# Kernel optimization log

Hardware: AMD Instinct MI355X
Metric: run time of the kernel (lower is better)

## Reference

```python
import jax, jax.numpy as jnp
import numpy as np

EPS = 1e-5
NEG = -1e20


def layer_norm(x, gamma, beta):
    mu = jnp.mean(x, axis=-1, keepdims=True)
    var = jnp.mean(jnp.square(x - mu), axis=-1, keepdims=True)
    return (x - mu) * jax.lax.rsqrt(var + EPS) * gamma + beta


def setup_inputs() -> dict:
    key = jax.random.key(0)
    ks = jax.random.split(key, 12)
    B, S, D, H, HD = 2, 2048, 1024, 16, 64
    hid = H * HD
    inp = {
        "q": jax.random.normal(ks[0], (B, S, D), jnp.float32),
        "k": jax.random.normal(ks[1], (B, S, D), jnp.float32),
        "v": jax.random.normal(ks[2], (B, S, D), jnp.float32),
        "mask": jax.random.randint(ks[3], (B, 1, S, S), 0, 2, jnp.int32),
        "Wq": jax.random.normal(ks[4], (D, hid), jnp.float32) * (D ** -0.5),
        "bq": jnp.zeros((hid,), jnp.float32),
        "Wk": jax.random.normal(ks[5], (D, hid), jnp.float32) * (D ** -0.5),
        "bk": jnp.zeros((hid,), jnp.float32),
        "Wv": jax.random.normal(ks[6], (D, hid), jnp.float32) * (D ** -0.5),
        "bv": jnp.zeros((hid,), jnp.float32),
        "Wo": jax.random.normal(ks[7], (hid, D), jnp.float32) * (hid ** -0.5),
        "bo": jnp.zeros((D,), jnp.float32),
        "gamma": jnp.ones((D,), jnp.float32),
        "beta": jnp.zeros((D,), jnp.float32),
    }
    return inp


def reference(q, k, v, mask, Wq, bq, Wk, bk, Wv, bv, Wo, bo, gamma, beta):
    B, S, D = q.shape
    H, HD = 16, 64
    scale = HD ** -0.5
    qh = (layer_norm(q, gamma, beta) @ Wq + bq).reshape(B, S, H, HD).transpose(0, 2, 1, 3)
    kh = (layer_norm(k, gamma, beta) @ Wk + bk).reshape(B, S, H, HD).transpose(0, 2, 1, 3)
    vh = (layer_norm(v, gamma, beta) @ Wv + bv).reshape(B, S, H, HD).transpose(0, 2, 1, 3)
    dots = jnp.einsum('bhqd,bhkd->bhqk', qh, kh)  # [B,H,S,S]
    dots = jnp.where(mask == 0, NEG, dots) * scale  # mask BEFORE scale (as in source)
    attn = jax.nn.softmax(dots, axis=-1)
    out = jnp.einsum('bhqk,bhkd->bhqd', attn, vh)  # [B,H,S,HD]
    # Faithful to `out.view(B, S, -1)` on a [B,H,S,HD]-contiguous tensor: raw reshape,
    # no head transpose.
    out = out.reshape(B, S, H * HD)
    return out @ Wo + bo
```

## Files before the change

### kernel.cpp

```cpp
#include <hip/hip_runtime.h>

typedef short short8 __attribute__((ext_vector_type(8)));
typedef float f32x4 __attribute__((ext_vector_type(4)));

#define QSCALE 0.18033688011112042f

__device__ __forceinline__ unsigned short f2bf(float f) {
  unsigned u = __builtin_bit_cast(unsigned, f);
  u += 0x7fffu + ((u >> 16) & 1u);
  return (unsigned short)(u >> 16);
}

__device__ __forceinline__ void gload16(const void* g, void* l) {
  typedef __attribute__((address_space(1))) unsigned int gas;
  typedef __attribute__((address_space(3))) unsigned int las;
  __builtin_amdgcn_global_load_lds((gas*)(unsigned long long)g,
                                   (las*)(unsigned)(unsigned long long)l, 16, 0, 0);
}

__device__ __forceinline__ short8 mk8(unsigned r0, unsigned r1, unsigned r2, unsigned r3) {
  union { unsigned u[4]; short8 s; } t;
  t.u[0] = r0; t.u[1] = r1; t.u[2] = r2; t.u[3] = r3;
  return t.s;
}

#define MFMA16(a, b, c) __builtin_amdgcn_mfma_f32_16x16x32_bf16(a, b, c, 0, 0, 0)

__global__ __launch_bounds__(256) void wtrans_kernel(
    const float* __restrict__ Wq, const float* __restrict__ Wk,
    const float* __restrict__ Wv, const float* __restrict__ Wo,
    unsigned short* __restrict__ Wt) {
  const int wsel = blockIdx.z;
  const float* W = wsel == 0 ? Wq : wsel == 1 ? Wk : wsel == 2 ? Wv : Wo;
  const float wscale = (wsel == 0) ? QSCALE : 1.0f;
  unsigned short* out = Wt + (long)wsel * 1048576;
  __shared__ float lds[64][65];
  const int t = threadIdx.x;
  const int k0 = blockIdx.x * 64, n0 = blockIdx.y * 64;
#pragma unroll
  for (int i = 0; i < 4; ++i) {
    int r = (t >> 4) + i * 16, c4 = (t & 15) * 4;
    float4 vv = *(const float4*)(W + (long)(k0 + r) * 1024 + n0 + c4);
    lds[r][c4] = vv.x; lds[r][c4 + 1] = vv.y; lds[r][c4 + 2] = vv.z; lds[r][c4 + 3] = vv.w;
  }
  __syncthreads();
#pragma unroll
  for (int i = 0; i < 16; ++i) {
    int flat = t + i * 256;
    int n = flat >> 6, kk = flat & 63;
    out[(long)(n0 + n) * 1024 + k0 + kk] = f2bf(lds[kk][n] * wscale);
  }
}

__global__ __launch_bounds__(256) void maskpack_kernel(const int* __restrict__ mask,
                                                       unsigned* __restrict__ bits) {
  const long n = 8388608;
  const long stride = (long)gridDim.x * 256;
  const int lane = threadIdx.x & 63;
  for (long i = (long)blockIdx.x * 256 + threadIdx.x; i < n; i += stride) {
    unsigned long long bal = __ballot(mask[i] != 0);
    if ((lane & 31) == 0) bits[i >> 5] = (unsigned)(bal >> (lane & 32));
  }
}

__global__ __launch_bounds__(256) void ln_kernel(
    const float* __restrict__ q, const float* __restrict__ k, const float* __restrict__ v,
    const float* __restrict__ gamma, const float* __restrict__ beta,
    unsigned short* __restrict__ lnq, unsigned short* __restrict__ lnk,
    unsigned short* __restrict__ lnv) {
  const int row = blockIdx.x, which = blockIdx.y;
  const float* x = (which == 0 ? q : which == 1 ? k : v) + (long)row * 1024;
  unsigned short* y = (which == 0 ? lnq : which == 1 ? lnk : lnv) + (long)row * 1024;
  const int t = threadIdx.x, lane = t & 63, wv = t >> 6;
  float4 xv = ((const float4*)x)[t];
  float s = xv.x + xv.y + xv.z + xv.w;
  float s2 = xv.x * xv.x + xv.y * xv.y + xv.z * xv.z + xv.w * xv.w;
#pragma unroll
  for (int off = 32; off > 0; off >>= 1) {
    s += __shfl_down(s, off);
    s2 += __shfl_down(s2, off);
  }
  __shared__ float red[8];
  if (lane == 0) { red[wv] = s; red[wv + 4] = s2; }
  __syncthreads();
  float tot = red[0] + red[1] + red[2] + red[3];
  float tot2 = red[4] + red[5] + red[6] + red[7];
  float mu = tot * (1.0f / 1024.0f);
  float var = tot2 * (1.0f / 1024.0f) - mu * mu;
  float rs = rsqrtf(var + 1e-5f);
  float4 g = ((const float4*)gamma)[t];
  float4 be = ((const float4*)beta)[t];
  ushort4 o;
  o.x = f2bf((xv.x - mu) * rs * g.x + be.x);
  o.y = f2bf((xv.y - mu) * rs * g.y + be.y);
  o.z = f2bf((xv.z - mu) * rs * g.z + be.z);
  o.w = f2bf((xv.w - mu) * rs * g.w + be.w);
  ((ushort4*)y)[t] = o;
}

template <int BM, int MODE>
__global__ __launch_bounds__(256) void gemm_kernel(
    const unsigned short* __restrict__ A0, const unsigned short* __restrict__ A1,
    const unsigned short* __restrict__ A2, const unsigned short* __restrict__ Wt,
    const float* __restrict__ b0, const float* __restrict__ b1,
    const float* __restrict__ b2, unsigned short* __restrict__ outB,
    unsigned short* __restrict__ outV, float* __restrict__ outF) {
  constexpr int MI = BM / 32;
  constexpr int NT = 32;
  constexpr int ACHA = BM / 64;
  const int z = blockIdx.z;
  const unsigned short* A = z == 0 ? A0 : z == 1 ? A1 : A2;
  const unsigned short* Bt = Wt + (long)z * 1048576;
  const float* bias = z == 0 ? b0 : z == 1 ? b1 : b2;
  unsigned short* outz = outB + (long)z * 4194304;
  const float bscale = (MODE == 0 && z == 0) ? QSCALE : 1.0f;

  __shared__ char lds[(BM + 128) * 128];
  char* As = lds;
  char* Bs = lds + BM * 128;
  const int tid = threadIdx.x, lane = tid & 63, w = tid >> 6;
  const int g = lane >> 4;
  const int wr = w >> 1, wc = w & 1;
  const int m0 = blockIdx.x * BM, n0 = blockIdx.y * 128;

  f32x4 acc[MI][4] = {};

#define GSTAGE(KT, BUF)                                                       \
  {                                                                           \
    _Pragma("unroll") for (int i = 0; i < ACHA; ++i) {                        \
      int cc = tid + i * 256;                                                 \
      int row = cc >> 2, p = cc & 3;                                          \
      int kk = p ^ ((row >> 1) & 3);                                          \
      gload16(A + (long)(m0 + row) * 1024 + (KT)*32 + kk * 8,                 \
              As + (BUF) * (BM * 64) + cc * 16);                              \
    }                                                                         \
    _Pragma("unroll") for (int i = 0; i < 2; ++i) {                           \
      int cc = tid + i * 256;                                                 \
      int row = cc >> 2, p = cc & 3;                                          \
      int kk = p ^ ((row >> 1) & 3);                                          \
      gload16(Bt + (long)(n0 + row) * 1024 + (KT)*32 + kk * 8,                \
              Bs + (BUF)*8192 + cc * 16);                                     \
    }                                                                         \
  }

  GSTAGE(0, 0);
  asm volatile("s_waitcnt vmcnt(0)" ::: "memory");
  __builtin_amdgcn_s_barrier();

  for (int kt = 0; kt < NT; ++kt) {
    const int cur = kt & 1;
    if (kt + 1 < NT) GSTAGE(kt + 1, cur ^ 1);
    short8 af[MI], bf[4];
#pragma unroll
    for (int mi = 0; mi < MI; ++mi) {
      int row = wr * (BM / 2) + mi * 16 + (lane & 15);
      int part = g ^ ((row >> 1) & 3);
      af[mi] = *(const short8*)(As + cur * (BM * 64) + row * 64 + part * 16);
    }
#pragma unroll
    for (int ni = 0; ni < 4; ++ni) {
      int row = wc * 64 + ni * 16 + (lane & 15);
      int part = g ^ ((row >> 1) & 3);
      bf[ni] = *(const short8*)(Bs + cur * 8192 + row * 64 + part * 16);
    }
    __builtin_amdgcn_s_setprio(1);
#pragma unroll
    for (int mi = 0; mi < MI; ++mi)
#pragma unroll
      for (int ni = 0; ni < 4; ++ni)
        acc[mi][ni] = MFMA16(af[mi], bf[ni], acc[mi][ni]);
    __builtin_amdgcn_s_setprio(0);
    asm volatile("s_waitcnt vmcnt(0) lgkmcnt(0)" ::: "memory");
    __builtin_amdgcn_s_barrier();
  }
#undef GSTAGE

#pragma unroll
  for (int mi = 0; mi < MI; ++mi) {
    int mbase = m0 + wr * (BM / 2) + mi * 16 + ((lane >> 4) << 2);
#pragma unroll
    for (int ni = 0; ni < 4; ++ni) {
      int j = n0 + wc * 64 + ni * 16 + (lane & 15);
      float bj = bias[j] * bscale;
      float t0 = acc[mi][ni][0] + bj;
      float t1 = acc[mi][ni][1] + bj;
      float t2 = acc[mi][ni][2] + bj;
      float t3 = acc[mi][ni][3] + bj;
      if constexpr (MODE == 0) {
        int b = mbase >> 11, s = mbase & 2047;
        int h = j >> 6, d = j & 63;
        if (z == 2) {
          unsigned lo, hi;
          asm("v_cvt_pk_bf16_f32 %0, %1, %2" : "=v"(lo) : "v"(t0), "v"(t1));
          asm("v_cvt_pk_bf16_f32 %0, %1, %2" : "=v"(hi) : "v"(t2), "v"(t3));
          uint2 o; o.x = lo; o.y = hi;
          int sp = (s & ~31) | (((s >> 2) & 3) << 3) | (((s >> 4) & 1) << 2);
          *(uint2*)(outV + ((long)(b * 16 + h) * 64 + d) * 2048 + sp) = o;
        } else {
          long base = (((long)(b * 16 + h)) * 2048 + s) * 64 + d;
          outz[base] = f2bf(t0);
          outz[base + 64] = f2bf(t1);
          outz[base + 128] = f2bf(t2);
          outz[base + 192] = f2bf(t3);
        }
      } else {
        outF[(long)mbase * 1024 + j] = t0;
        outF[(long)(mbase + 1) * 1024 + j] = t1;
        outF[(long)(mbase + 2) * 1024 + j] = t2;
        outF[(long)(mbase + 3) * 1024 + j] = t3;
      }
    }
  }
}

__global__ __launch_bounds__(256, 4) void attn_kernel(
    const unsigned short* __restrict__ qh, const unsigned short* __restrict__ kh,
    const unsigned short* __restrict__ vt, const unsigned* __restrict__ mbits,
    unsigned short* __restrict__ O) {
  constexpr int S = 2048, NT = 32;
  __shared__ char lds[32768];
  char* Ks = lds;
  char* Vts = lds + 16384;
  const int tid = threadIdx.x, lane = tid & 63, w = tid >> 6;
  const int g = lane >> 4, c = lane & 15;

  const int flat = blockIdx.y * 32 + blockIdx.x;
  const int fl2 = (flat & 7) * 128 + (flat >> 3);
  const int qb = fl2 & 31, bh = fl2 >> 5, b = bh >> 4;
  const int kt0 = (fl2 & 3) * 8;

  const unsigned short* qp = qh + (long)bh * S * 64;
  const unsigned short* kp = kh + (long)bh * S * 64;
  const unsigned short* vp = vt + (long)bh * 64 * S;
  unsigned short* op = O + (long)bh * S * 64;
  const unsigned* mrow = mbits + (long)b * S * 64;
  const int q0 = qb * 64 + w * 16;
  const int myq = q0 + c;

  short8 bq_[2];
#pragma unroll
  for (int ds = 0; ds < 2; ++ds)
    bq_[ds] = *(const short8*)(qp + (long)myq * 64 + ds * 32 + g * 8);

  f32x4 o_acc[4] = {};
  float lpart = 0.f;

#define STAGE(KT, BUF)                                                              \
  {                                                                                 \
    _Pragma("unroll") for (int i = 0; i < 2; ++i) {                                 \
      int cc = tid + i * 256;                                                       \
      int row = cc >> 3, pg = (cc & 7) ^ (row & 7);                                 \
      gload16(kp + (long)((KT)*64 + row) * 64 + pg * 8, Ks + (BUF)*8192 + cc * 16); \
    }                                                                               \
    _Pragma("unroll") for (int i = 0; i < 2; ++i) {                                 \
      int cc = tid + i * 256;                                                       \
      int row = cc >> 3, pg = (cc & 7) ^ (row & 7);                                 \
      gload16(vp + (long)row * S + (KT)*64 + pg * 8, Vts + (BUF)*8192 + cc * 16);   \
    }                                                                               \
  }

  STAGE(kt0, 0);
  uint2 mcur = *(const uint2*)(mrow + (long)myq * 64 + kt0 * 2);
  uint2 mnxt = mcur;

  for (int kt = 0; kt < NT; ++kt) {
    const int cur = kt & 1;
    if (kt + 1 < NT) {
      const int nx = (kt0 + kt + 1) & 31;
      STAGE(nx, cur ^ 1);
      mnxt = *(const uint2*)(mrow + (long)myq * 64 + nx * 2);
      asm volatile("s_waitcnt vmcnt(5)" ::: "memory");
    } else {
      asm volatile("s_waitcnt vmcnt(0)" ::: "memory");
    }
    __builtin_amdgcn_s_barrier();

    f32x4 sc[4] = {};
    const char* Kb = Ks + cur * 8192;
    __builtin_amdgcn_s_setprio(1);
#pragma unroll
    for (int ds = 0; ds < 2; ++ds) {
#pragma unroll
      for (int kf = 0; kf < 4; ++kf) {
        int row = kf * 16 + c;
        int part = (ds * 4 + g) ^ (row & 7);
        short8 ak = *(const short8*)(Kb + row * 128 + part * 16);
        sc[kf] = MFMA16(ak, bq_[ds], sc[kf]);
      }
    }
    __builtin_amdgcn_s_setprio(0);

    unsigned ws0 = mcur.x >> (g * 4), ws1 = mcur.y >> (g * 4);
    unsigned pw[8];
#pragma unroll
    for (int kf = 0; kf < 4; ++kf) {
      unsigned wsh = ((kf >= 2) ? ws1 : ws0) >> ((kf & 1) * 16);
      float pv0 = __builtin_amdgcn_exp2f(sc[kf][0]);
      float pv1 = __builtin_amdgcn_exp2f(sc[kf][1]);
      float pv2 = __builtin_amdgcn_exp2f(sc[kf][2]);
      float pv3 = __builtin_amdgcn_exp2f(sc[kf][3]);
      pv0 = (wsh & 1u) ? pv0 : 0.f;
      pv1 = (wsh & 2u) ? pv1 : 0.f;
      pv2 = (wsh & 4u) ? pv2 : 0.f;
      pv3 = (wsh & 8u) ? pv3 : 0.f;
      lpart += (pv0 + pv1) + (pv2 + pv3);
      asm("v_cvt_pk_bf16_f32 %0, %1, %2" : "=v"(pw[kf * 2]) : "v"(pv0), "v"(pv1));
      asm("v_cvt_pk_bf16_f32 %0, %1, %2" : "=v"(pw[kf * 2 + 1]) : "v"(pv2), "v"(pv3));
    }
    short8 pa0 = mk8(pw[0], pw[1], pw[2], pw[3]);
    short8 pa1 = mk8(pw[4], pw[5], pw[6], pw[7]);
    mcur = mnxt;

    const char* Vb = Vts + cur * 8192;
    __builtin_amdgcn_s_setprio(1);
#pragma unroll
    for (int ks = 0; ks < 2; ++ks) {
      short8 pa = ks ? pa1 : pa0;
      int part = ks * 4 + g;
#pragma unroll
      for (int nd = 0; nd < 4; ++nd) {
        int d = nd * 16 + c;
        short8 bv = *(const short8*)(Vb + d * 128 + ((part ^ (d & 7)) * 16));
        o_acc[nd] = MFMA16(pa, bv, o_acc[nd]);
      }
    }
    __builtin_amdgcn_s_setprio(0);

    asm volatile("s_waitcnt lgkmcnt(0)" ::: "memory");
    __builtin_amdgcn_sched_barrier(0);
    __builtin_amdgcn_s_barrier();
  }
#undef STAGE

  lpart += __shfl_xor(lpart, 16);
  lpart += __shfl_xor(lpart, 32);
#pragma unroll
  for (int r = 0; r < 4; ++r) {
    float lr = __shfl(lpart, g * 4 + r);
    float inv = 1.0f / lr;
    int qrow = q0 + g * 4 + r;
#pragma unroll
    for (int nd = 0; nd < 4; ++nd)
      op[(long)qrow * 64 + nd * 16 + c] = f2bf(o_acc[nd][r] * inv);
  }
}

extern "C" void kernel_launch(void* const* d_in, const int* in_sizes, int n_in,
                              void* d_out, int out_size, void* d_ws, size_t ws_size,
                              hipStream_t stream) {
  const float* q = (const float*)d_in[0];
  const float* k = (const float*)d_in[1];
  const float* v = (const float*)d_in[2];
  const int* mask = (const int*)d_in[3];
  const float* Wq = (const float*)d_in[4];
  const float* bq = (const float*)d_in[5];
  const float* Wk = (const float*)d_in[6];
  const float* bk = (const float*)d_in[7];
  const float* Wv = (const float*)d_in[8];
  const float* bv = (const float*)d_in[9];
  const float* Wo = (const float*)d_in[10];
  const float* bo = (const float*)d_in[11];
  const float* gamma = (const float*)d_in[12];
  const float* beta = (const float*)d_in[13];
  float* out = (float*)d_out;

  char* ws = (char*)d_ws;
  unsigned short* Wt = (unsigned short*)ws;
  unsigned* mbits = (unsigned*)(ws + 8u * 1024 * 1024);
  unsigned short* lnq = (unsigned short*)(ws + 9u * 1024 * 1024);
  unsigned short* lnk = lnq + 4194304;
  unsigned short* lnv = lnk + 4194304;
  unsigned short* qh = lnv + 4194304;
  unsigned short* kh = qh + 4194304;
  unsigned short* vtb = kh + 4194304;
  unsigned short* Ob = lnq;

  wtrans_kernel<<<dim3(16, 16, 4), 256, 0, stream>>>(Wq, Wk, Wv, Wo, Wt);
  maskpack_kernel<<<1024, 256, 0, stream>>>(mask, mbits);
  ln_kernel<<<dim3(4096, 3), 256, 0, stream>>>(q, k, v, gamma, beta, lnq, lnk, lnv);
  gemm_kernel<128, 0><<<dim3(32, 8, 3), 256, 0, stream>>>(lnq, lnk, lnv, Wt, bq, bk, bv,
                                                          qh, vtb, nullptr);
  attn_kernel<<<dim3(32, 32), 256, 0, stream>>>(qh, kh, vtb, mbits, Ob);
  gemm_kernel<64, 1><<<dim3(64, 8, 1), 256, 0, stream>>>(Ob, Ob, Ob, Wt + 3 * 1048576,
                                                         bo, bo, bo, nullptr, nullptr, out);
}
```

Measured before the change: 142.6 us.

## Double query rows per attention wave to reuse K/V tiles across two MFMA groups

```diff
diff --git a/kernel.cpp b/kernel.cpp
--- a/kernel.cpp
+++ b/kernel.cpp
@@ -213,7 +213,7 @@
   }
 }
 
-__global__ __launch_bounds__(256, 4) void attn_kernel(
+__global__ __launch_bounds__(256, 2) void attn_kernel(
     const unsigned short* __restrict__ qh, const unsigned short* __restrict__ kh,
     const unsigned short* __restrict__ vt, const unsigned* __restrict__ mbits,
     unsigned short* __restrict__ O) {
@@ -224,9 +224,9 @@
   const int tid = threadIdx.x, lane = tid & 63, w = tid >> 6;
   const int g = lane >> 4, c = lane & 15;
 
-  const int flat = blockIdx.y * 32 + blockIdx.x;
-  const int fl2 = (flat & 7) * 128 + (flat >> 3);
-  const int qb = fl2 & 31, bh = fl2 >> 5, b = bh >> 4;
+  const int flat = blockIdx.y * 16 + blockIdx.x;
+  const int fl2 = (flat & 7) * 64 + (flat >> 3);
+  const int qb = fl2 & 15, bh = fl2 >> 4, b = bh >> 4;
   const int kt0 = (fl2 & 3) * 8;
 
   const unsigned short* qp = qh + (long)bh * S * 64;
@@ -234,16 +234,18 @@
   const unsigned short* vp = vt + (long)bh * 64 * S;
   unsigned short* op = O + (long)bh * S * 64;
   const unsigned* mrow = mbits + (long)b * S * 64;
-  const int q0 = qb * 64 + w * 16;
-  const int myq = q0 + c;
-
-  short8 bq_[2];
-#pragma unroll
-  for (int ds = 0; ds < 2; ++ds)
-    bq_[ds] = *(const short8*)(qp + (long)myq * 64 + ds * 32 + g * 8);
-
-  f32x4 o_acc[4] = {};
-  float lpart = 0.f;
+  const int q0 = qb * 128 + w * 32;
+  const int myq0 = q0 + c, myq1 = q0 + 16 + c;
+
+  short8 bq_[2][2];
+#pragma unroll
+  for (int qg = 0; qg < 2; ++qg)
+#pragma unroll
+    for (int ds = 0; ds < 2; ++ds)
+      bq_[qg][ds] = *(const short8*)(qp + (long)(q0 + qg * 16 + c) * 64 + ds * 32 + g * 8);
+
+  f32x4 o_acc[2][4] = {};
+  float lp0 = 0.f, lp1 = 0.f;
 
 #define STAGE(KT, BUF)                                                              \
   {                                                                                 \
@@ -259,23 +261,47 @@
     }                                                                               \
   }
 
+#define SOFTMAX(SC, MC, LP, PA0, PA1)                                               \
+  {                                                                                 \
+    unsigned ws0 = MC.x >> (g * 4), ws1 = MC.y >> (g * 4);                          \
+    unsigned pw[8];                                                                 \
+    _Pragma("unroll") for (int kf = 0; kf < 4; ++kf) {                              \
+      unsigned wsh = ((kf >= 2) ? ws1 : ws0) >> ((kf & 1) * 16);                    \
+      float pv0 = __builtin_amdgcn_exp2f(SC[kf][0]);                                \
+      float pv1 = __builtin_amdgcn_exp2f(SC[kf][1]);                                \
+      float pv2 = __builtin_amdgcn_exp2f(SC[kf][2]);                                \
+      float pv3 = __builtin_amdgcn_exp2f(SC[kf][3]);                                \
+      pv0 = (wsh & 1u) ? pv0 : 0.f;                                                 \
+      pv1 = (wsh & 2u) ? pv1 : 0.f;                                                 \
+      pv2 = (wsh & 4u) ? pv2 : 0.f;                                                 \
+      pv3 = (wsh & 8u) ? pv3 : 0.f;                                                 \
+      LP += (pv0 + pv1) + (pv2 + pv3);                                              \
+      asm("v_cvt_pk_bf16_f32 %0, %1, %2" : "=v"(pw[kf * 2]) : "v"(pv0), "v"(pv1));  \
+      asm("v_cvt_pk_bf16_f32 %0, %1, %2" : "=v"(pw[kf * 2 + 1]) : "v"(pv2), "v"(pv3)); \
+    }                                                                               \
+    PA0 = mk8(pw[0], pw[1], pw[2], pw[3]);                                          \
+    PA1 = mk8(pw[4], pw[5], pw[6], pw[7]);                                          \
+  }
+
   STAGE(kt0, 0);
-  uint2 mcur = *(const uint2*)(mrow + (long)myq * 64 + kt0 * 2);
-  uint2 mnxt = mcur;
+  uint2 m0c = *(const uint2*)(mrow + (long)myq0 * 64 + kt0 * 2);
+  uint2 m1c = *(const uint2*)(mrow + (long)myq1 * 64 + kt0 * 2);
+  uint2 m0n, m1n;
 
   for (int kt = 0; kt < NT; ++kt) {
     const int cur = kt & 1;
     if (kt + 1 < NT) {
       const int nx = (kt0 + kt + 1) & 31;
       STAGE(nx, cur ^ 1);
-      mnxt = *(const uint2*)(mrow + (long)myq * 64 + nx * 2);
-      asm volatile("s_waitcnt vmcnt(5)" ::: "memory");
+      m0n = *(const uint2*)(mrow + (long)myq0 * 64 + nx * 2);
+      m1n = *(const uint2*)(mrow + (long)myq1 * 64 + nx * 2);
+      asm volatile("s_waitcnt vmcnt(6)" ::: "memory");
     } else {
       asm volatile("s_waitcnt vmcnt(0)" ::: "memory");
     }
     __builtin_amdgcn_s_barrier();
 
-    f32x4 sc[4] = {};
+    f32x4 sc0[4] = {}, sc1[4] = {};
     const char* Kb = Ks + cur * 8192;
     __builtin_amdgcn_s_setprio(1);
 #pragma unroll
@@ -285,43 +311,31 @@
         int row = kf * 16 + c;
         int part = (ds * 4 + g) ^ (row & 7);
         short8 ak = *(const short8*)(Kb + row * 128 + part * 16);
-        sc[kf] = MFMA16(ak, bq_[ds], sc[kf]);
+        sc0[kf] = MFMA16(ak, bq_[0][ds], sc0[kf]);
+        sc1[kf] = MFMA16(ak, bq_[1][ds], sc1[kf]);
       }
     }
     __builtin_amdgcn_s_setprio(0);
 
-    unsigned ws0 = mcur.x >> (g * 4), ws1 = mcur.y >> (g * 4);
-    unsigned pw[8];
-#pragma unroll
-    for (int kf = 0; kf < 4; ++kf) {
-      unsigned wsh = ((kf >= 2) ? ws1 : ws0) >> ((kf & 1) * 16);
-      float pv0 = __builtin_amdgcn_exp2f(sc[kf][0]);
-      float pv1 = __builtin_amdgcn_exp2f(sc[kf][1]);
-      float pv2 = __builtin_amdgcn_exp2f(sc[kf][2]);
-      float pv3 = __builtin_amdgcn_exp2f(sc[kf][3]);
-      pv0 = (wsh & 1u) ? pv0 : 0.f;
-      pv1 = (wsh & 2u) ? pv1 : 0.f;
-      pv2 = (wsh & 4u) ? pv2 : 0.f;
-      pv3 = (wsh & 8u) ? pv3 : 0.f;
-      lpart += (pv0 + pv1) + (pv2 + pv3);
-      asm("v_cvt_pk_bf16_f32 %0, %1, %2" : "=v"(pw[kf * 2]) : "v"(pv0), "v"(pv1));
-      asm("v_cvt_pk_bf16_f32 %0, %1, %2" : "=v"(pw[kf * 2 + 1]) : "v"(pv2), "v"(pv3));
-    }
-    short8 pa0 = mk8(pw[0], pw[1], pw[2], pw[3]);
-    short8 pa1 = mk8(pw[4], pw[5], pw[6], pw[7]);
-    mcur = mnxt;
+    short8 pa00, pa01, pa10, pa11;
+    SOFTMAX(sc0, m0c, lp0, pa00, pa01);
+    SOFTMAX(sc1, m1c, lp1, pa10, pa11);
+    m0c = m0n;
+    m1c = m1n;
 
     const char* Vb = Vts + cur * 8192;
     __builtin_amdgcn_s_setprio(1);
 #pragma unroll
     for (int ks = 0; ks < 2; ++ks) {
-      short8 pa = ks ? pa1 : pa0;
+      short8 paA = ks ? pa01 : pa00;
+      short8 paB = ks ? pa11 : pa10;
       int part = ks * 4 + g;
 #pragma unroll
       for (int nd = 0; nd < 4; ++nd) {
         int d = nd * 16 + c;
         short8 bv = *(const short8*)(Vb + d * 128 + ((part ^ (d & 7)) * 16));
-        o_acc[nd] = MFMA16(pa, bv, o_acc[nd]);
+        o_acc[0][nd] = MFMA16(paA, bv, o_acc[0][nd]);
+        o_acc[1][nd] = MFMA16(paB, bv, o_acc[1][nd]);
       }
     }
     __builtin_amdgcn_s_setprio(0);
@@ -330,18 +344,26 @@
     __builtin_amdgcn_sched_barrier(0);
     __builtin_amdgcn_s_barrier();
   }
+#undef SOFTMAX
 #undef STAGE
 
-  lpart += __shfl_xor(lpart, 16);
-  lpart += __shfl_xor(lpart, 32);
+  lp0 += __shfl_xor(lp0, 16);
+  lp0 += __shfl_xor(lp0, 32);
+  lp1 += __shfl_xor(lp1, 16);
+  lp1 += __shfl_xor(lp1, 32);
 #pragma unroll
   for (int r = 0; r < 4; ++r) {
-    float lr = __shfl(lpart, g * 4 + r);
-    float inv = 1.0f / lr;
-    int qrow = q0 + g * 4 + r;
-#pragma unroll
-    for (int nd = 0; nd < 4; ++nd)
-      op[(long)qrow * 64 + nd * 16 + c] = f2bf(o_acc[nd][r] * inv);
+    float lr0 = __shfl(lp0, g * 4 + r);
+    float lr1 = __shfl(lp1, g * 4 + r);
+    float inv0 = 1.0f / lr0;
+    float inv1 = 1.0f / lr1;
+    int qrow0 = q0 + g * 4 + r;
+    int qrow1 = q0 + 16 + g * 4 + r;
+#pragma unroll
+    for (int nd = 0; nd < 4; ++nd) {
+      op[(long)qrow0 * 64 + nd * 16 + c] = f2bf(o_acc[0][nd][r] * inv0);
+      op[(long)qrow1 * 64 + nd * 16 + c] = f2bf(o_acc[1][nd][r] * inv1);
+    }
   }
 }
 
@@ -380,7 +402,7 @@
   ln_kernel<<<dim3(4096, 3), 256, 0, stream>>>(q, k, v, gamma, beta, lnq, lnk, lnv);
   gemm_kernel<128, 0><<<dim3(32, 8, 3), 256, 0, stream>>>(lnq, lnk, lnv, Wt, bq, bk, bv,
                                                           qh, vtb, nullptr);
-  attn_kernel<<<dim3(32, 32), 256, 0, stream>>>(qh, kh, vtb, mbits, Ob);
+  attn_kernel<<<dim3(16, 32), 256, 0, stream>>>(qh, kh, vtb, mbits, Ob);
   gemm_kernel<64, 1><<<dim3(64, 8, 1), 256, 0, stream>>>(Ob, Ob, Ob, Wt + 3 * 1048576,
                                                          bo, bo, bo, nullptr, nullptr, out);
 }
```

Result: faster. 139.1 us (-2.5%).
